# Optimization experiments

Measured on AMD Instinct MI355X. Metric: run time of the kernel, lower is better.

The kernel has to match this reference:

```python
import jax, jax.numpy as jnp
import numpy as np

RANK, N, T, S = 8, 64, 64, 64
IN_F, OUT_F = N * T, N * S  # 4096, 4096


def setup_inputs() -> dict:
    key = jax.random.key(0)
    k1, k2, k3, k4 = jax.random.split(key, 4)
    scale = 1.0 / np.sqrt(IN_F)
    x = jax.random.normal(k1, (8, 2048, IN_F), dtype=jnp.float32)
    A = jax.random.normal(k2, (RANK, N, T), dtype=jnp.float32) * scale
    B = jax.random.normal(k3, (RANK, S, N), dtype=jnp.float32) * scale
    bias = jax.random.uniform(k4, (OUT_F,), dtype=jnp.float32, minval=-scale, maxval=scale)
    return {"x": x, "A": A, "B": B, "bias": bias}


def reference(x, A, B, bias):
    # Kronecker-product weight reconstruction: sum over rank b of
    # W[i*S+k, j*N+m] = sum_b A[b,i,j] * B[b,k,m]
    W = jnp.einsum('bij,bkm->ikjm', A, B).reshape(OUT_F, IN_F)
    # F.linear: x @ W.T + bias
    return jnp.einsum('bsi,oi->bso', x, W) + bias
```

## Files before the change

### kernel.cpp

```cpp
#include <hip/hip_runtime.h>
#include <hip/hip_bf16.h>
#include <stdint.h>

#define M_DIM 16384
#define N_DIM 4096
#define K_DIM 4096

typedef short short8 __attribute__((ext_vector_type(8)));
typedef unsigned short ushort8 __attribute__((ext_vector_type(8)));
typedef float f32x4 __attribute__((ext_vector_type(4)));

__device__ __forceinline__ unsigned short f2b(float f) {
    union { float f; uint32_t u; } v; v.f = f;
    return (unsigned short)((v.u + 0x7FFFu + ((v.u >> 16) & 1u)) >> 16);
}

__device__ __forceinline__ void async_ld16(const void* g, void* l) {
    __builtin_amdgcn_global_load_lds(
        (const __attribute__((address_space(1))) uint32_t*)g,
        (__attribute__((address_space(3))) uint32_t*)l, 16, 0, 0);
}

__global__ __launch_bounds__(256) void build_w_kernel(
    const float* __restrict__ A, const float* __restrict__ B,
    unsigned short* __restrict__ W)
{
    size_t idx = ((size_t)blockIdx.x * 256 + threadIdx.x) * 8;
    int o = (int)(idx >> 12);
    int c = (int)(idx & 4095);
    int i = o >> 6, k = o & 63;
    int j = c >> 6, m0 = c & 63;

    float acc[8];
#pragma unroll
    for (int t = 0; t < 8; ++t) acc[t] = 0.0f;
#pragma unroll
    for (int b = 0; b < 8; ++b) {
        float a = A[b * 4096 + i * 64 + j];
        const float4* bp = (const float4*)&B[b * 4096 + k * 64 + m0];
        float4 b0 = bp[0], b1 = bp[1];
        acc[0] += a * b0.x; acc[1] += a * b0.y;
        acc[2] += a * b0.z; acc[3] += a * b0.w;
        acc[4] += a * b1.x; acc[5] += a * b1.y;
        acc[6] += a * b1.z; acc[7] += a * b1.w;
    }
    ushort8 r;
#pragma unroll
    for (int t = 0; t < 8; ++t) r[t] = f2b(acc[t]);
    *(ushort8*)&W[idx] = r;
}

__global__ __launch_bounds__(256) void cvt_x_kernel(
    const float* __restrict__ x, unsigned short* __restrict__ xb)
{
    size_t idx = ((size_t)blockIdx.x * 256 + threadIdx.x) * 8;
    const float4* gp = (const float4*)&x[idx];
    float4 v0 = gp[0], v1 = gp[1];
    ushort8 r;
    r[0] = f2b(v0.x); r[1] = f2b(v0.y); r[2] = f2b(v0.z); r[3] = f2b(v0.w);
    r[4] = f2b(v1.x); r[5] = f2b(v1.y); r[6] = f2b(v1.z); r[7] = f2b(v1.w);
    *(ushort8*)&xb[idx] = r;
}

template <bool PRECONV>
__global__ __launch_bounds__(256, 2) void gemm_kernel(
    const float* __restrict__ xf,
    const unsigned short* __restrict__ xb,
    const unsigned short* __restrict__ W,
    const float* __restrict__ bias,
    float* __restrict__ out)
{
    __shared__ unsigned short As[128 * 32];
    __shared__ unsigned short Bs[128 * 32];

    const int tid = threadIdx.x;
    const int wave = tid >> 6;
    const int lane = tid & 63;
    const int quad = lane >> 4;
    const int l15 = lane & 15;
    const int wm = (wave >> 1) * 64;
    const int wn = (wave & 1) * 64;
    const size_t mbase = (size_t)blockIdx.y * 128;
    const int nbase = blockIdx.x * 128;

    f32x4 acc[4][4];
#pragma unroll
    for (int a = 0; a < 4; ++a)
#pragma unroll
        for (int b = 0; b < 4; ++b)
            acc[a][b] = (f32x4){0.0f, 0.0f, 0.0f, 0.0f};

    for (int k0 = 0; k0 < K_DIM; k0 += 32) {
        {
            const int issue0 = wave * 2;
#pragma unroll
            for (int t = 0; t < 2; ++t) {
                const int isn = issue0 + t;
                const int row = isn * 16 + (lane >> 2);
                const int kc = (lane & 3) * 8;
                async_ld16(&W[(size_t)(nbase + row) * K_DIM + k0 + kc],
                           &Bs[isn * 512]);
            }
        }
        if (PRECONV) {
            const int issue0 = wave * 2;
#pragma unroll
            for (int t = 0; t < 2; ++t) {
                const int isn = issue0 + t;
                const int row = isn * 16 + (lane >> 2);
                const int kc = (lane & 3) * 8;
                async_ld16(&xb[(mbase + row) * K_DIM + k0 + kc],
                           &As[isn * 512]);
            }
        } else {
            const int row = tid >> 1;
            const int half = tid & 1;
            const float* gp = xf + (mbase + row) * K_DIM + k0 + half * 16;
            float4 v0 = ((const float4*)gp)[0];
            float4 v1 = ((const float4*)gp)[1];
            float4 v2 = ((const float4*)gp)[2];
            float4 v3 = ((const float4*)gp)[3];
            ushort8 lo, hi;
            lo[0] = f2b(v0.x); lo[1] = f2b(v0.y); lo[2] = f2b(v0.z); lo[3] = f2b(v0.w);
            lo[4] = f2b(v1.x); lo[5] = f2b(v1.y); lo[6] = f2b(v1.z); lo[7] = f2b(v1.w);
            hi[0] = f2b(v2.x); hi[1] = f2b(v2.y); hi[2] = f2b(v2.z); hi[3] = f2b(v2.w);
            hi[4] = f2b(v3.x); hi[5] = f2b(v3.y); hi[6] = f2b(v3.z); hi[7] = f2b(v3.w);
            *(ushort8*)&As[row * 32 + half * 16] = lo;
            *(ushort8*)&As[row * 32 + half * 16 + 8] = hi;
        }
        __syncthreads();

        short8 af[4], bf[4];
#pragma unroll
        for (int mt = 0; mt < 4; ++mt)
            af[mt] = *(const short8*)&As[(wm + mt * 16 + l15) * 32 + quad * 8];
#pragma unroll
        for (int nt = 0; nt < 4; ++nt)
            bf[nt] = *(const short8*)&Bs[(wn + nt * 16 + l15) * 32 + quad * 8];
#pragma unroll
        for (int mt = 0; mt < 4; ++mt)
#pragma unroll
            for (int nt = 0; nt < 4; ++nt)
                acc[mt][nt] = __builtin_amdgcn_mfma_f32_16x16x32_bf16(
                    af[mt], bf[nt], acc[mt][nt], 0, 0, 0);
        __syncthreads();
    }

    float bv[4];
#pragma unroll
    for (int nt = 0; nt < 4; ++nt) bv[nt] = bias[nbase + wn + nt * 16 + l15];
#pragma unroll
    for (int mt = 0; mt < 4; ++mt) {
#pragma unroll
        for (int r = 0; r < 4; ++r) {
            const size_t row = mbase + wm + mt * 16 + quad * 4 + r;
            float* orow = out + row * N_DIM + nbase + wn + l15;
#pragma unroll
            for (int nt = 0; nt < 4; ++nt)
                orow[nt * 16] = acc[mt][nt][r] + bv[nt];
        }
    }
}

extern "C" void kernel_launch(void* const* d_in, const int* in_sizes, int n_in,
                              void* d_out, int out_size, void* d_ws, size_t ws_size,
                              hipStream_t stream)
{
    const float* x = (const float*)d_in[0];
    const float* A = (const float*)d_in[1];
    const float* B = (const float*)d_in[2];
    const float* bias = (const float*)d_in[3];
    float* out = (float*)d_out;

    unsigned short* Wb = (unsigned short*)d_ws;
    const size_t wbytes = (size_t)N_DIM * K_DIM * 2;
    const size_t xbytes = (size_t)M_DIM * K_DIM * 2;

    build_w_kernel<<<(N_DIM * (size_t)K_DIM) / 8 / 256, 256, 0, stream>>>(A, B, Wb);

    if (ws_size >= wbytes + xbytes) {
        unsigned short* xbuf = (unsigned short*)((char*)d_ws + wbytes);
        cvt_x_kernel<<<((size_t)M_DIM * K_DIM) / 8 / 256, 256, 0, stream>>>(x, xbuf);
        gemm_kernel<true><<<dim3(N_DIM / 128, M_DIM / 128), 256, 0, stream>>>(
            nullptr, xbuf, Wb, bias, out);
    } else {
        gemm_kernel<false><<<dim3(N_DIM / 128, M_DIM / 128), 256, 0, stream>>>(
            x, nullptr, Wb, bias, out);
    }
}
```

Measured before the change: 1.038 ms.

## Add 256x256-tile bf16 GEMM with 4-stage async LDS pipeline and swizzle

Replaces the pre-converted-input path's 128x128 GEMM with a 512-thread kernel that computes 256x256 output tiles. It uses a 4-slot ring of LDS buffers filled by async global-to-LDS loads three tiles ahead, tracked with explicit vmcnt waits. It also adds an XOR swizzle on the K chunks to avoid LDS bank conflicts, s_setprio around the MFMA bursts, and a block-index remap for cache locality. The aim is more data reuse per tile and overlap of global loads with MFMA work; in exchange it uses about 128KB of LDS per block, which limits occupancy to one block per CU, and hand-tuned wait counts that are fragile.

```diff
diff --git a/kernel.cpp b/kernel.cpp
--- a/kernel.cpp
+++ b/kernel.cpp
@@ -1,10 +1,10 @@
 #include <hip/hip_runtime.h>
-#include <hip/hip_bf16.h>
 #include <stdint.h>
 
 #define M_DIM 16384
 #define N_DIM 4096
 #define K_DIM 4096
+#define KTILES (K_DIM / 32)
 
 typedef short short8 __attribute__((ext_vector_type(8)));
 typedef unsigned short ushort8 __attribute__((ext_vector_type(8)));
@@ -20,6 +20,9 @@
         (const __attribute__((address_space(1))) uint32_t*)g,
         (__attribute__((address_space(3))) uint32_t*)l, 16, 0, 0);
 }
+
+#define VMCNT(n) asm volatile("s_waitcnt vmcnt(" #n ")" ::: "memory")
+#define LGKM0    asm volatile("s_waitcnt lgkmcnt(0)" ::: "memory")
 
 __global__ __launch_bounds__(256) void build_w_kernel(
     const float* __restrict__ A, const float* __restrict__ B,
@@ -62,10 +65,121 @@
     *(ushort8*)&xb[idx] = r;
 }
 
-template <bool PRECONV>
-__global__ __launch_bounds__(256, 2) void gemm_kernel(
+__global__ __launch_bounds__(512, 2) void gemm256_kernel(
+    const unsigned short* __restrict__ xb,
+    const unsigned short* __restrict__ W,
+    const float* __restrict__ bias,
+    float* __restrict__ out)
+{
+    __shared__ __align__(16) unsigned short AsB[4][256 * 32];
+    __shared__ __align__(16) unsigned short BsB[4][256 * 32];
+
+    const int tid = threadIdx.x;
+    const int wave = tid >> 6;
+    const int lane = tid & 63;
+    const int quad = lane >> 4;
+    const int l15 = lane & 15;
+    const int wr = wave >> 2;
+    const int wc = wave & 3;
+
+    const int wg = ((blockIdx.x & 7) << 7) | (blockIdx.x >> 3);
+    const size_t mbase = (size_t)(wg >> 4) * 256;
+    const int nbase = (wg & 15) * 256;
+
+    const int arow0 = wr * 128 + l15;
+    const int brow0 = wc * 64 + l15;
+
+    f32x4 acc[8][4];
+#pragma unroll
+    for (int a = 0; a < 8; ++a)
+#pragma unroll
+        for (int b = 0; b < 4; ++b)
+            acc[a][b] = (f32x4){0.0f, 0.0f, 0.0f, 0.0f};
+
+    auto stage_half = [&](int tile, int li) {
+        const int slot = tile & 3;
+        const int f = li * 512 + tid;
+        const int row = f >> 2;
+        const int kof = tile * 32 + ((((f & 3) ^ ((row >> 1) & 3))) << 3);
+        unsigned short* ab = &AsB[slot][(li * 512 + wave * 64) * 8];
+        unsigned short* bb = &BsB[slot][(li * 512 + wave * 64) * 8];
+        async_ld16(&xb[(mbase + row) * K_DIM + kof], ab);
+        async_ld16(&W[(size_t)(nbase + row) * K_DIM + kof], bb);
+    };
+    auto frag = [&](const unsigned short* buf, int row) -> short8 {
+        return *(const short8*)&buf[row * 32 + ((quad ^ ((row >> 1) & 3)) << 3)];
+    };
+
+    stage_half(0, 0); stage_half(0, 1);
+    stage_half(1, 0); stage_half(1, 1);
+    stage_half(2, 0); stage_half(2, 1);
+    VMCNT(8);
+    __builtin_amdgcn_s_barrier();
+
+#pragma unroll 1
+    for (int t = 0; t < KTILES; ++t) {
+        const unsigned short* As_c = AsB[t & 3];
+        const unsigned short* Bs_c = BsB[t & 3];
+        const bool pf = (t + 3) < KTILES;
+
+        short8 af[4], bf[4];
+#pragma unroll
+        for (int mt = 0; mt < 4; ++mt) af[mt] = frag(As_c, arow0 + mt * 16);
+#pragma unroll
+        for (int nt = 0; nt < 4; ++nt) bf[nt] = frag(Bs_c, brow0 + nt * 16);
+        if (pf) stage_half(t + 3, 0);
+        __builtin_amdgcn_s_barrier();
+        LGKM0;
+        __builtin_amdgcn_sched_barrier(0);
+        __builtin_amdgcn_s_setprio(1);
+#pragma unroll
+        for (int mt = 0; mt < 4; ++mt)
+#pragma unroll
+            for (int nt = 0; nt < 4; ++nt)
+                acc[mt][nt] = __builtin_amdgcn_mfma_f32_16x16x32_bf16(
+                    af[mt], bf[nt], acc[mt][nt], 0, 0, 0);
+        __builtin_amdgcn_s_setprio(0);
+        __builtin_amdgcn_s_barrier();
+
+        short8 ag[4];
+#pragma unroll
+        for (int mt = 0; mt < 4; ++mt) ag[mt] = frag(As_c, arow0 + 64 + mt * 16);
+        if (pf) stage_half(t + 3, 1);
+        __builtin_amdgcn_s_barrier();
+        LGKM0;
+        __builtin_amdgcn_sched_barrier(0);
+        __builtin_amdgcn_s_setprio(1);
+#pragma unroll
+        for (int mt = 0; mt < 4; ++mt)
+#pragma unroll
+            for (int nt = 0; nt < 4; ++nt)
+                acc[4 + mt][nt] = __builtin_amdgcn_mfma_f32_16x16x32_bf16(
+                    ag[mt], bf[nt], acc[4 + mt][nt], 0, 0, 0);
+        __builtin_amdgcn_s_setprio(0);
+        if (t < KTILES - 3)       { VMCNT(8); }
+        else if (t == KTILES - 3) { VMCNT(4); }
+        else                      { VMCNT(0); }
+        __builtin_amdgcn_s_barrier();
+    }
+
+    float bv[4];
+#pragma unroll
+    for (int nt = 0; nt < 4; ++nt) bv[nt] = bias[nbase + wc * 64 + nt * 16 + l15];
+#pragma unroll
+    for (int mt = 0; mt < 8; ++mt) {
+#pragma unroll
+        for (int r = 0; r < 4; ++r) {
+            const size_t row = mbase + wr * 128 + mt * 16 + quad * 4 + r;
+            float* orow = out + row * N_DIM + nbase + wc * 64 + l15;
+#pragma unroll
+            for (int nt = 0; nt < 4; ++nt)
+                orow[nt * 16] = acc[mt][nt][r] + bv[nt];
+        }
+    }
+}
+
+__global__ __launch_bounds__(256, 2) void gemm128_f32(
     const float* __restrict__ xf,
-    const unsigned short* __restrict__ xb,
     const unsigned short* __restrict__ W,
     const float* __restrict__ bias,
     float* __restrict__ out)
@@ -102,17 +216,7 @@
                            &Bs[isn * 512]);
             }
         }
-        if (PRECONV) {
-            const int issue0 = wave * 2;
-#pragma unroll
-            for (int t = 0; t < 2; ++t) {
-                const int isn = issue0 + t;
-                const int row = isn * 16 + (lane >> 2);
-                const int kc = (lane & 3) * 8;
-                async_ld16(&xb[(mbase + row) * K_DIM + k0 + kc],
-                           &As[isn * 512]);
-            }
-        } else {
+        {
             const int row = tid >> 1;
             const int half = tid & 1;
             const float* gp = xf + (mbase + row) * K_DIM + k0 + half * 16;
@@ -181,10 +285,8 @@
     if (ws_size >= wbytes + xbytes) {
         unsigned short* xbuf = (unsigned short*)((char*)d_ws + wbytes);
         cvt_x_kernel<<<((size_t)M_DIM * K_DIM) / 8 / 256, 256, 0, stream>>>(x, xbuf);
-        gemm_kernel<true><<<dim3(N_DIM / 128, M_DIM / 128), 256, 0, stream>>>(
-            nullptr, xbuf, Wb, bias, out);
+        gemm256_kernel<<<dim3(1024), 512, 0, stream>>>(xbuf, Wb, bias, out);
     } else {
-        gemm_kernel<false><<<dim3(N_DIM / 128, M_DIM / 128), 256, 0, stream>>>(
-            x, nullptr, Wb, bias, out);
-    }
-}
+        gemm128_f32<<<dim3(N_DIM / 128, M_DIM / 128), 256, 0, stream>>>(x, Wb, bias, out);
+    }
+}
```

After: 1.050 ms. No clear change (+1.2%).
